# Optimization experiments

Measured on AMD Instinct MI355X. Metric: run time of the kernel, lower is better.

## Reference

```python
import jax, jax.numpy as jnp
import numpy as np

B, S, E, A = 4, 4096, 512, 64

def setup_inputs() -> dict:
    key = jax.random.key(0)
    ks = jax.random.split(key, 9)
    return {
        "query": jax.random.normal(ks[0], (B, S, E), dtype=jnp.float32),
        "key":   jax.random.normal(ks[1], (B, S, E), dtype=jnp.float32),
        "value": jax.random.normal(ks[2], (B, S, E), dtype=jnp.float32),
        "Wq": jax.random.normal(ks[3], (E, A), dtype=jnp.float32) / np.sqrt(E),
        "bq": jax.random.normal(ks[4], (A,), dtype=jnp.float32) * 0.01,
        "Wk": jax.random.normal(ks[5], (E, A), dtype=jnp.float32) / np.sqrt(E),
        "bk": jax.random.normal(ks[6], (A,), dtype=jnp.float32) * 0.01,
        "Wv": jax.random.normal(ks[7], (E, A), dtype=jnp.float32) / np.sqrt(E),
        "bv": jax.random.normal(ks[8], (A,), dtype=jnp.float32) * 0.01,
        "look_ahead_mask": 1,
    }

def reference(query, key, value, Wq, bq, Wk, bk, Wv, bv, look_ahead_mask):
    # Linear projections (torch Linear: x @ W^T + b; here W stored as [in,out])
    q = query @ Wq + bq            # [B,S,A]
    k = key   @ Wk + bk            # [B,S,A]
    v = value @ Wv + bv            # [B,S,A]
    scale = jnp.sqrt(jnp.asarray(A, dtype=q.dtype))
    qk = jnp.einsum('bsa,bta->bst', q, k) / scale   # [B,S,S]
    if look_ahead_mask:
        # faithful to source: MULTIPLICATIVE tril mask (not additive -inf)
        tril = jnp.tril(jnp.ones((qk.shape[-1], qk.shape[-1]), dtype=qk.dtype))
        qk = qk * tril
    attn = jax.nn.softmax(qk, axis=-1)              # [B,S,S]
    return jnp.einsum('bst,bta->bsa', attn, v)       # [B,S,A]
```

## Files before the change

### kernel.cpp

```cpp
#include <hip/hip_runtime.h>
#include <cstdint>

constexpr int BB = 4, SS = 4096, EE = 512, AA = 64;
constexpr int NT = 64;
constexpr int NSLOT = 272;

typedef __bf16 bf16x8 __attribute__((ext_vector_type(8)));
typedef float  f32x4  __attribute__((ext_vector_type(4)));
typedef float  f4     __attribute__((ext_vector_type(4)));
typedef unsigned short u16x4 __attribute__((ext_vector_type(4)));
typedef unsigned short u16x8 __attribute__((ext_vector_type(8)));

#define MFMA16(a, b, c) __builtin_amdgcn_mfma_f32_16x16x32_bf16((a), (b), (c), 0, 0, 0)

typedef const void __attribute__((address_space(1))) gvoid_t;
typedef void __attribute__((address_space(3))) lvoid_t;
__device__ __forceinline__ void gload16(const void* g, void* l) {
    __builtin_amdgcn_global_load_lds((gvoid_t*)g, (lvoid_t*)l, 16, 0, 0);
}

__device__ __forceinline__ unsigned short f2bf(float x) {
    union { float f; unsigned u; } v; v.f = x;
    unsigned r = v.u + 0x7fffu + ((v.u >> 16) & 1u);
    return (unsigned short)(r >> 16);
}
__device__ __forceinline__ float bf2f(unsigned short h) {
    union { unsigned u; float f; } v; v.u = ((unsigned)h) << 16;
    return v.f;
}
__device__ __forceinline__ unsigned short f2bfc(float x) {
    __bf16 h = (__bf16)x;
    return __builtin_bit_cast(unsigned short, h);
}
__device__ __forceinline__ bf16x8 as_bf16x8(u16x8 u) {
    union { u16x8 u; bf16x8 b; } v; v.u = u; return v.b;
}

__global__ void split_w_kernel(const float* __restrict__ Wq,
                               const float* __restrict__ Wk,
                               const float* __restrict__ Wv,
                               unsigned short* __restrict__ wt_h,
                               unsigned short* __restrict__ wt_l) {
    int idx = blockIdx.x * blockDim.x + threadIdx.x;
    if (idx >= 3 * EE * AA) return;
    int t = idx / (EE * AA);
    int rem = idx - t * (EE * AA);
    int k = rem >> 6;
    int n = rem & 63;
    const float* W = (t == 0) ? Wq : (t == 1) ? Wk : Wv;
    float x = W[k * AA + n];
    unsigned short h = f2bf(x);
    unsigned short l = f2bf(x - bf2f(h));
    int o = (t * AA + n) * EE + k;
    wt_h[o] = h;
    wt_l[o] = l;
}

__launch_bounds__(128)
__global__ void proj_kernel(const float* __restrict__ Xq,
                            const float* __restrict__ Xk,
                            const float* __restrict__ Xv,
                            const float* __restrict__ bq,
                            const float* __restrict__ bk,
                            const float* __restrict__ bv,
                            const unsigned short* __restrict__ wt_h,
                            const unsigned short* __restrict__ wt_l,
                            unsigned short* __restrict__ q_hi,
                            unsigned short* __restrict__ q_lo,
                            unsigned short* __restrict__ kv) {
    const int t = blockIdx.y;
    const float* X    = (t == 0) ? Xq : (t == 1) ? Xk : Xv;
    const float* bias = (t == 0) ? bq : (t == 1) ? bk : bv;
    const int row0 = blockIdx.x * 32;
    const int tid = threadIdx.x;
    const int lane = tid & 63, w = tid >> 6;
    const int l15 = lane & 15, l4 = lane >> 4;

    __shared__ __align__(16) char smem[24576];

    f32x4 acc[4];
#pragma unroll
    for (int j = 0; j < 4; ++j) acc[j] = (f32x4){0.f, 0.f, 0.f, 0.f};

    const unsigned short* wtH = wt_h + t * AA * EE;
    const unsigned short* wtL = wt_l + t * AA * EE;

    for (int kc0 = 0; kc0 < EE; kc0 += 64) {
#pragma unroll
        for (int s = 0; s < 4; ++s) {
            int r = s * 8 + (tid >> 4);
            int c4 = (tid & 15) ^ (r & 7);
            gload16(X + (size_t)(row0 + r) * EE + kc0 + c4 * 4,
                    smem + s * 2048 + tid * 16);
        }
#pragma unroll
        for (int s = 0; s < 4; ++s) {
            int n = s * 16 + (tid >> 3);
            int cg = (tid & 7) ^ (n & 7);
            gload16(wtH + n * EE + kc0 + cg * 8,
                    smem + 8192 + s * 2048 + tid * 16);
            gload16(wtL + n * EE + kc0 + cg * 8,
                    smem + 16384 + s * 2048 + tid * 16);
        }
        asm volatile("s_waitcnt vmcnt(0)" ::: "memory");
        __syncthreads();

#pragma unroll
        for (int kc = 0; kc < 2; ++kc) {
            int r = w * 16 + l15;
            int c4a = (kc * 8 + l4 * 2) ^ (r & 7);
            int c4b = (kc * 8 + l4 * 2 + 1) ^ (r & 7);
            f4 va = *(const f4*)(smem + r * 256 + c4a * 16);
            f4 vb = *(const f4*)(smem + r * 256 + c4b * 16);
            u16x8 ahu, alu;
#pragma unroll
            for (int jj = 0; jj < 4; ++jj) {
                __bf16 h0 = (__bf16)va[jj];
                ahu[jj] = __builtin_bit_cast(unsigned short, h0);
                alu[jj] = f2bfc(va[jj] - (float)h0);
                __bf16 h1 = (__bf16)vb[jj];
                ahu[jj + 4] = __builtin_bit_cast(unsigned short, h1);
                alu[jj + 4] = f2bfc(vb[jj] - (float)h1);
            }
            bf16x8 a_h = as_bf16x8(ahu), a_l = as_bf16x8(alu);
#pragma unroll
            for (int j = 0; j < 4; ++j) {
                int n = j * 16 + l15;
                int byteB = n * 128 + (((kc * 4 + l4) ^ (n & 7)) << 4);
                bf16x8 b_h = as_bf16x8(*(const u16x8*)(smem + 8192 + byteB));
                bf16x8 b_l = as_bf16x8(*(const u16x8*)(smem + 16384 + byteB));
                acc[j] = MFMA16(a_h, b_h, acc[j]);
                acc[j] = MFMA16(a_h, b_l, acc[j]);
                acc[j] = MFMA16(a_l, b_h, acc[j]);
            }
        }
        __syncthreads();
    }

    float* stage = (float*)smem;
#pragma unroll
    for (int j = 0; j < 4; ++j) {
        int n = j * 16 + l15;
        float bv_ = bias[n];
#pragma unroll
        for (int reg = 0; reg < 4; ++reg) {
            int r = w * 16 + l4 * 4 + reg;
            stage[r * 65 + n] = acc[j][reg] + bv_;
        }
    }
    __syncthreads();

    if (t == 0) {
        int row = tid >> 2, n0 = (tid & 3) * 16;
        u16x8 h0, l0, h1, l1;
#pragma unroll
        for (int k = 0; k < 8; ++k) {
            float v = stage[row * 65 + n0 + k] * 0.125f;
            __bf16 hh = (__bf16)v;
            h0[k] = __builtin_bit_cast(unsigned short, hh);
            l0[k] = f2bfc(v - (float)hh);
        }
#pragma unroll
        for (int k = 0; k < 8; ++k) {
            float v = stage[row * 65 + n0 + 8 + k] * 0.125f;
            __bf16 hh = (__bf16)v;
            h1[k] = __builtin_bit_cast(unsigned short, hh);
            l1[k] = f2bfc(v - (float)hh);
        }
        size_t o = (size_t)(row0 + row) * AA + n0;
        *(u16x8*)(q_hi + o) = h0; *(u16x8*)(q_hi + o + 8) = h1;
        *(u16x8*)(q_lo + o) = l0; *(u16x8*)(q_lo + o + 8) = l1;
    } else {
        const int bb = row0 >> 12, kt = (row0 & 4095) >> 6;
        const int hb = (row0 >> 5) & 1;
        const size_t base = ((size_t)(bb * NT + kt) << 14) + (t == 2 ? 8192 : 0);
        const int ff = tid >> 5;
#pragma unroll
        for (int p = 0; p < 2; ++p) {
            int lane2 = (tid & 31) * 2 + p;
            u16x8 h, l;
            int f;
            if (t == 1) {
                f = (ff >> 1) * 4 + 2 * hb + (ff & 1);
                int n0 = (f >> 2) * 32 + (lane2 >> 4) * 8;
                int tt = (f & 3) * 16 + (lane2 & 15);
                int sr = tt & 31;
#pragma unroll
                for (int jj = 0; jj < 8; ++jj) {
                    float v = stage[sr * 65 + n0 + jj];
                    __bf16 hh = (__bf16)v;
                    h[jj] = __builtin_bit_cast(unsigned short, hh);
                    l[jj] = f2bfc(v - (float)hh);
                }
            } else {
                f = 4 * hb + ff;
                int n = (f & 3) * 16 + (lane2 & 15);
                int tt0 = (lane2 >> 4) * 8;
#pragma unroll
                for (int jj = 0; jj < 8; ++jj) {
                    float v = stage[(tt0 + jj) * 65 + n];
                    __bf16 hh = (__bf16)v;
                    h[jj] = __builtin_bit_cast(unsigned short, hh);
                    l[jj] = f2bfc(v - (float)hh);
                }
            }
            size_t o = base + (size_t)f * 512 + lane2 * 8;
            *(u16x8*)(kv + o) = h;
            *(u16x8*)(kv + o + 4096) = l;
        }
    }
}

__launch_bounds__(64)
__global__ void sufv_kernel(const unsigned short* __restrict__ kv,
                            float* __restrict__ sufv) {
    const int b = blockIdx.x >> 6;
    const int a = blockIdx.x & 63;
    const int t = threadIdx.x;
    __shared__ float sums[64];
    const size_t tb = ((size_t)(b * NT + t) << 14) + 8192;
    const int j = a >> 4, l15i = a & 15;
    float s = 0.f;
#pragma unroll
    for (int c2 = 0; c2 < 2; ++c2) {
#pragma unroll
        for (int l4i = 0; l4i < 4; ++l4i) {
            size_t off = tb + (((c2 * 4 + j) * 64 + l4i * 16 + l15i) << 3);
            u16x8 h = *(const u16x8*)(kv + off);
            u16x8 l = *(const u16x8*)(kv + off + 4096);
#pragma unroll
            for (int q = 0; q < 8; ++q) s += bf2f(h[q]) + bf2f(l[q]);
        }
    }
    sums[t] = s;
    __syncthreads();
    float suf = 0.f;
    for (int jj = t + 1; jj < 64; ++jj) suf += sums[jj];
    sufv[((size_t)(b * 64 + a)) * 64 + t] = suf;
}

__launch_bounds__(512)
__global__ void attn_chunk_kernel(const unsigned short* __restrict__ q_hi,
                                  const unsigned short* __restrict__ q_lo,
                                  const unsigned short* __restrict__ kv,
                                  float* __restrict__ facc_part,
                                  float* __restrict__ l_part) {
    const int idx = (int)blockIdx.x;
    const int b = idx & 3;
    const int s = (NSLOT - 1) - (idx >> 2);
    int k = (int)sqrtf((float)s + 0.5f);
    while (k * k > s) --k;
    while ((k + 1) * (k + 1) <= s) ++k;
    int i, c;
    if (s < k * (k + 1)) { i = 2 * k - 1; c = s - k * k; }
    else                 { i = 2 * k;     c = s - k * (k + 1); }
    const int t_begin = c * 4;
    const int tmax = 2 * i + 2;
    const int t_end = (t_begin + 4 < tmax) ? t_begin + 4 : tmax;

    const int tid = threadIdx.x;
    const int lane = tid & 63, w = tid >> 6;
    const int l15 = lane & 15, l4 = lane >> 4;

    __shared__ __align__(16) unsigned short kvbuf[16384];
    __shared__ __align__(16) unsigned short plds[8][1024];

    bf16x8 qh[2], ql[2];
    {
        size_t qrow = (size_t)(b * SS + i * 128 + w * 16 + l15) * AA;
#pragma unroll
        for (int kc = 0; kc < 2; ++kc) {
            qh[kc] = as_bf16x8(*(const u16x8*)(q_hi + qrow + kc * 32 + l4 * 8));
            ql[kc] = as_bf16x8(*(const u16x8*)(q_lo + qrow + kc * 32 + l4 * 8));
        }
    }

    f32x4 facc[4];
#pragma unroll
    for (int j = 0; j < 4; ++j) facc[j] = (f32x4){0.f, 0.f, 0.f, 0.f};
    float lsum = 0.f;

    const char* lb = (const char*)kvbuf;
    const int qbase = i * 128 + w * 16;

    for (int kt = t_begin; kt < t_end; ++kt) {
        {
            const char* gt = (const char*)kv + (((size_t)(b * NT + kt)) << 15) + tid * 16;
            char* lw = (char*)kvbuf + tid * 16;
#pragma unroll
            for (int p = 0; p < 4; ++p) gload16(gt + p * 8192, lw + p * 8192);
        }
        asm volatile("s_waitcnt vmcnt(0)" ::: "memory");
        __syncthreads();

        f32x4 sc[4];
#pragma unroll
        for (int j = 0; j < 4; ++j) sc[j] = (f32x4){0.f, 0.f, 0.f, 0.f};
        __builtin_amdgcn_s_setprio(1);
#pragma unroll
        for (int kc = 0; kc < 2; ++kc) {
#pragma unroll
            for (int j2 = 0; j2 < 4; ++j2) {
                int f = kc * 4 + j2;
                bf16x8 h = as_bf16x8(*(const u16x8*)(lb + f * 1024 + lane * 16));
                bf16x8 l = as_bf16x8(*(const u16x8*)(lb + 8192 + f * 1024 + lane * 16));
                sc[j2] = MFMA16(h, qh[kc], sc[j2]);
                sc[j2] = MFMA16(l, qh[kc], sc[j2]);
                sc[j2] = MFMA16(h, ql[kc], sc[j2]);
            }
        }
        __builtin_amdgcn_s_setprio(0);

        const int dq = qbase - 64 * kt;
        const bool anyMask = (dq < 63);
#pragma unroll
        for (int j2 = 0; j2 < 4; ++j2) {
            u16x4 p4;
#pragma unroll
            for (int reg = 0; reg < 4; ++reg) {
                float sv_ = sc[j2][reg];
                if (anyMask) {
                    int tl = j2 * 16 + l4 * 4 + reg;
                    if (tl > dq + l15) sv_ = 0.f;
                }
                float p = __expf(sv_);
                lsum += p;
                p4[reg] = f2bf(p);
            }
            int byte = (l15 * 128 + j2 * 32 + l4 * 8) ^ ((l15 & 7) << 4);
            *(u16x4*)((char*)plds[w] + byte) = p4;
        }

        __builtin_amdgcn_s_setprio(1);
#pragma unroll
        for (int c2 = 0; c2 < 2; ++c2) {
            int byteA = (l15 * 128 + c2 * 64 + l4 * 16) ^ ((l15 & 7) << 4);
            bf16x8 pf = as_bf16x8(*(const u16x8*)((const char*)plds[w] + byteA));
#pragma unroll
            for (int j = 0; j < 4; ++j) {
                int f = c2 * 4 + j;
                bf16x8 vh = as_bf16x8(*(const u16x8*)(lb + 16384 + f * 1024 + lane * 16));
                bf16x8 vl = as_bf16x8(*(const u16x8*)(lb + 24576 + f * 1024 + lane * 16));
                facc[j] = MFMA16(pf, vh, facc[j]);
                facc[j] = MFMA16(pf, vl, facc[j]);
            }
        }
        __builtin_amdgcn_s_setprio(0);

        if (kt + 1 < t_end) __syncthreads();
    }

    {
        float rs = lsum;
        rs += __shfl_xor(rs, 16);
        rs += __shfl_xor(rs, 32);
        const size_t slot = (size_t)b * NSLOT + s;
        if (l4 == 0)
            l_part[slot * 128 + w * 16 + l15] = rs;

        float* fp = facc_part + slot * 8192;
#pragma unroll
        for (int j = 0; j < 4; ++j) {
#pragma unroll
            for (int reg = 0; reg < 4; ++reg) {
                int row = w * 16 + l4 * 4 + reg, a = j * 16 + l15;
                fp[row * 64 + a] = facc[j][reg];
            }
        }
    }
}

__launch_bounds__(256)
__global__ void combine_kernel(const float* __restrict__ facc_part,
                               const float* __restrict__ l_part,
                               const float* __restrict__ sufv,
                               float* __restrict__ out) {
    const int i64 = blockIdx.x;
    const int b = blockIdx.y;
    const int tid = threadIdx.x;
    const int i128 = i64 >> 1;
    const int nch = (i128 >> 1) + 1;
    const int k2 = i128 >> 1;
    const int C = (i128 & 1) ? (k2 + 1) * (k2 + 1) : k2 * (k2 + 1);
    const size_t slot0 = (size_t)b * NSLOT + C;
    const int rbase = (i64 & 1) * 64;
    __shared__ float linv[64];
    __shared__ float sv[64];
    if (tid < 64) {
        float l = 64.0f * (float)(NT - 2 * i128 - 2);
        for (int cc = 0; cc < nch; ++cc)
            l += l_part[(slot0 + cc) * 128 + rbase + tid];
        linv[tid] = 1.f / l;
        sv[tid] = sufv[((size_t)(b * 64 + tid)) * 64 + (2 * i128 + 1)];
    }
    __syncthreads();
    float* ob = out + ((size_t)(b * SS + i64 * 64)) * AA;
#pragma unroll
    for (int k = 0; k < 4; ++k) {
        int e = (tid + k * 256) * 4;
        int row = e >> 6, a = e & 63;
        f4 acc = {sv[a], sv[a + 1], sv[a + 2], sv[a + 3]};
        for (int cc = 0; cc < nch; ++cc) {
            f4 v = *(const f4*)(facc_part + (slot0 + cc) * 8192 + (rbase + row) * 64 + a);
            acc += v;
        }
        acc *= linv[row];
        *(f4*)(ob + e) = acc;
    }
}

extern "C" void kernel_launch(void* const* d_in, const int* in_sizes, int n_in,
                              void* d_out, int out_size, void* d_ws, size_t ws_size,
                              hipStream_t stream) {
    const float* query = (const float*)d_in[0];
    const float* key   = (const float*)d_in[1];
    const float* value = (const float*)d_in[2];
    const float* Wq    = (const float*)d_in[3];
    const float* bq    = (const float*)d_in[4];
    const float* Wk    = (const float*)d_in[5];
    const float* bk    = (const float*)d_in[6];
    const float* Wv    = (const float*)d_in[7];
    const float* bv    = (const float*)d_in[8];

    char* ws = (char*)d_ws;
    const size_t MB = 1u << 20;
    unsigned short* q_hi = (unsigned short*)(ws + 0 * MB);
    unsigned short* q_lo = (unsigned short*)(ws + 2 * MB);
    unsigned short* kv   = (unsigned short*)(ws + 4 * MB);
    float* sufv      = (float*)(ws + 12 * MB);
    float* l_part    = (float*)(ws + 13 * MB);
    float* facc_part = (float*)(ws + 14 * MB);
    unsigned short* wt_h = (unsigned short*)(ws + 52 * MB);
    unsigned short* wt_l = wt_h + 3 * AA * EE;

    split_w_kernel<<<(3 * EE * AA + 255) / 256, 256, 0, stream>>>(Wq, Wk, Wv, wt_h, wt_l);
    proj_kernel<<<dim3(BB * SS / 32, 3), 128, 0, stream>>>(
        query, key, value, bq, bk, bv, wt_h, wt_l, q_hi, q_lo, kv);
    sufv_kernel<<<BB * AA, 64, 0, stream>>>(kv, sufv);
    attn_chunk_kernel<<<dim3(4 * NSLOT, 1), 512, 0, stream>>>(
        q_hi, q_lo, kv, facc_part, l_part);
    combine_kernel<<<dim3(NT, BB), 256, 0, stream>>>(facc_part, l_part, sufv, (float*)d_out);
}
```

Before: 94.75 us.

## Double K-chunk in projection and batch two KV tiles per sync in attention

The projection kernel now stages 128-wide K chunks per iteration, doubling its shared memory to halve the number of load/sync rounds. The attention kernel loads two consecutive KV tiles into a doubled LDS buffer with one wait and barrier, then processes both through a macro-expanded tile body. The aim is fewer global-load round trips and barriers. In exchange LDS use per block grows, which may reduce occupancy.

Measured after the change: 95.34 us. About the same (+0.6%).

```diff
diff --git a/kernel.cpp b/kernel.cpp
--- a/kernel.cpp
+++ b/kernel.cpp
@@ -76,7 +76,7 @@
     const int lane = tid & 63, w = tid >> 6;
     const int l15 = lane & 15, l4 = lane >> 4;
 
-    __shared__ __align__(16) char smem[24576];
+    __shared__ __align__(16) char smem[49152];
 
     f32x4 acc[4];
 #pragma unroll
@@ -85,33 +85,33 @@
     const unsigned short* wtH = wt_h + t * AA * EE;
     const unsigned short* wtL = wt_l + t * AA * EE;
 
-    for (int kc0 = 0; kc0 < EE; kc0 += 64) {
-#pragma unroll
-        for (int s = 0; s < 4; ++s) {
-            int r = s * 8 + (tid >> 4);
-            int c4 = (tid & 15) ^ (r & 7);
-            gload16(X + (size_t)(row0 + r) * EE + kc0 + c4 * 4,
-                    smem + s * 2048 + tid * 16);
-        }
-#pragma unroll
-        for (int s = 0; s < 4; ++s) {
-            int n = s * 16 + (tid >> 3);
-            int cg = (tid & 7) ^ (n & 7);
-            gload16(wtH + n * EE + kc0 + cg * 8,
-                    smem + 8192 + s * 2048 + tid * 16);
-            gload16(wtL + n * EE + kc0 + cg * 8,
-                    smem + 16384 + s * 2048 + tid * 16);
+    for (int kc0 = 0; kc0 < EE; kc0 += 128) {
+#pragma unroll
+        for (int s = 0; s < 8; ++s) {
+            int e = s * 128 + tid;
+            int r = e >> 5, g = e & 31;
+            int cg = g ^ (r & 7);
+            gload16(X + (size_t)(row0 + r) * EE + kc0 + cg * 4,
+                    smem + e * 16);
+        }
+#pragma unroll
+        for (int s = 0; s < 8; ++s) {
+            int e = s * 128 + tid;
+            int n = e >> 4, g = e & 15;
+            int cg = g ^ (n & 7);
+            gload16(wtH + n * EE + kc0 + cg * 8, smem + 16384 + e * 16);
+            gload16(wtL + n * EE + kc0 + cg * 8, smem + 32768 + e * 16);
         }
         asm volatile("s_waitcnt vmcnt(0)" ::: "memory");
         __syncthreads();
 
 #pragma unroll
-        for (int kc = 0; kc < 2; ++kc) {
+        for (int kc = 0; kc < 4; ++kc) {
             int r = w * 16 + l15;
-            int c4a = (kc * 8 + l4 * 2) ^ (r & 7);
-            int c4b = (kc * 8 + l4 * 2 + 1) ^ (r & 7);
-            f4 va = *(const f4*)(smem + r * 256 + c4a * 16);
-            f4 vb = *(const f4*)(smem + r * 256 + c4b * 16);
+            int g0 = (kc * 8 + l4 * 2) ^ (r & 7);
+            int g1 = (kc * 8 + l4 * 2 + 1) ^ (r & 7);
+            f4 va = *(const f4*)(smem + r * 512 + g0 * 16);
+            f4 vb = *(const f4*)(smem + r * 512 + g1 * 16);
             u16x8 ahu, alu;
 #pragma unroll
             for (int jj = 0; jj < 4; ++jj) {
@@ -126,9 +126,9 @@
 #pragma unroll
             for (int j = 0; j < 4; ++j) {
                 int n = j * 16 + l15;
-                int byteB = n * 128 + (((kc * 4 + l4) ^ (n & 7)) << 4);
-                bf16x8 b_h = as_bf16x8(*(const u16x8*)(smem + 8192 + byteB));
-                bf16x8 b_l = as_bf16x8(*(const u16x8*)(smem + 16384 + byteB));
+                int byteB = n * 256 + (((kc * 4 + l4) ^ (n & 7)) << 4);
+                bf16x8 b_h = as_bf16x8(*(const u16x8*)(smem + 16384 + byteB));
+                bf16x8 b_l = as_bf16x8(*(const u16x8*)(smem + 32768 + byteB));
                 acc[j] = MFMA16(a_h, b_h, acc[j]);
                 acc[j] = MFMA16(a_h, b_l, acc[j]);
                 acc[j] = MFMA16(a_l, b_h, acc[j]);
@@ -238,6 +238,56 @@
     for (int jj = t + 1; jj < 64; ++jj) suf += sums[jj];
     sufv[((size_t)(b * 64 + a)) * 64 + t] = suf;
 }
+
+#define ATTN_TILE(LB, KT)                                                      \
+  do {                                                                         \
+    const char* lb = (LB);                                                     \
+    f32x4 sc[4];                                                               \
+    _Pragma("unroll") for (int j = 0; j < 4; ++j)                              \
+        sc[j] = (f32x4){0.f, 0.f, 0.f, 0.f};                                   \
+    __builtin_amdgcn_s_setprio(1);                                             \
+    _Pragma("unroll") for (int kc = 0; kc < 2; ++kc) {                         \
+      _Pragma("unroll") for (int j2 = 0; j2 < 4; ++j2) {                       \
+        int f = kc * 4 + j2;                                                   \
+        bf16x8 h = as_bf16x8(*(const u16x8*)(lb + f * 1024 + lane * 16));      \
+        bf16x8 l = as_bf16x8(*(const u16x8*)(lb + 8192 + f * 1024 + lane * 16));\
+        sc[j2] = MFMA16(h, qh[kc], sc[j2]);                                    \
+        sc[j2] = MFMA16(l, qh[kc], sc[j2]);                                    \
+        sc[j2] = MFMA16(h, ql[kc], sc[j2]);                                    \
+      }                                                                        \
+    }                                                                          \
+    __builtin_amdgcn_s_setprio(0);                                             \
+    const int dq = qbase - 64 * (KT);                                          \
+    const bool anyMask = (dq < 63);                                            \
+    _Pragma("unroll") for (int j2 = 0; j2 < 4; ++j2) {                         \
+      u16x4 p4;                                                                \
+      _Pragma("unroll") for (int reg = 0; reg < 4; ++reg) {                    \
+        float sv_ = sc[j2][reg];                                               \
+        if (anyMask) {                                                         \
+          int tl = j2 * 16 + l4 * 4 + reg;                                     \
+          if (tl > dq + l15) sv_ = 0.f;                                        \
+        }                                                                      \
+        float p = __expf(sv_);                                                 \
+        lsum += p;                                                             \
+        p4[reg] = f2bf(p);                                                     \
+      }                                                                        \
+      int byte = (l15 * 128 + j2 * 32 + l4 * 8) ^ ((l15 & 7) << 4);            \
+      *(u16x4*)((char*)plds[w] + byte) = p4;                                   \
+    }                                                                          \
+    __builtin_amdgcn_s_setprio(1);                                             \
+    _Pragma("unroll") for (int c2 = 0; c2 < 2; ++c2) {                         \
+      int byteA = (l15 * 128 + c2 * 64 + l4 * 16) ^ ((l15 & 7) << 4);          \
+      bf16x8 pf = as_bf16x8(*(const u16x8*)((const char*)plds[w] + byteA));    \
+      _Pragma("unroll") for (int j = 0; j < 4; ++j) {                          \
+        int f = c2 * 4 + j;                                                    \
+        bf16x8 vh = as_bf16x8(*(const u16x8*)(lb + 16384 + f * 1024 + lane * 16));\
+        bf16x8 vl = as_bf16x8(*(const u16x8*)(lb + 24576 + f * 1024 + lane * 16));\
+        facc[j] = MFMA16(pf, vh, facc[j]);                                     \
+        facc[j] = MFMA16(pf, vl, facc[j]);                                     \
+      }                                                                        \
+    }                                                                          \
+    __builtin_amdgcn_s_setprio(0);                                             \
+  } while (0)
 
 __launch_bounds__(512)
 __global__ void attn_chunk_kernel(const unsigned short* __restrict__ q_hi,
@@ -262,7 +312,7 @@
     const int lane = tid & 63, w = tid >> 6;
     const int l15 = lane & 15, l4 = lane >> 4;
 
-    __shared__ __align__(16) unsigned short kvbuf[16384];
+    __shared__ __align__(16) unsigned short kvbuf[2][16384];
     __shared__ __align__(16) unsigned short plds[8][1024];
 
     bf16x8 qh[2], ql[2];
@@ -280,74 +330,28 @@
     for (int j = 0; j < 4; ++j) facc[j] = (f32x4){0.f, 0.f, 0.f, 0.f};
     float lsum = 0.f;
 
-    const char* lb = (const char*)kvbuf;
     const int qbase = i * 128 + w * 16;
-
-    for (int kt = t_begin; kt < t_end; ++kt) {
+    const char* gbase = (const char*)kv + (((size_t)(b * NT)) << 15) + tid * 16;
+
+    for (int kt = t_begin; kt < t_end; kt += 2) {
+        const int np = (kt + 1 < t_end) ? 2 : 1;
         {
-            const char* gt = (const char*)kv + (((size_t)(b * NT + kt)) << 15) + tid * 16;
-            char* lw = (char*)kvbuf + tid * 16;
+            const char* gt = gbase + (((size_t)kt) << 15);
+            char* lw = (char*)kvbuf[0] + tid * 16;
 #pragma unroll
             for (int p = 0; p < 4; ++p) gload16(gt + p * 8192, lw + p * 8192);
+            if (np == 2) {
+#pragma unroll
+                for (int p = 4; p < 8; ++p) gload16(gt + p * 8192, lw + p * 8192);
+            }
         }
         asm volatile("s_waitcnt vmcnt(0)" ::: "memory");
         __syncthreads();
 
-        f32x4 sc[4];
-#pragma unroll
-        for (int j = 0; j < 4; ++j) sc[j] = (f32x4){0.f, 0.f, 0.f, 0.f};
-        __builtin_amdgcn_s_setprio(1);
-#pragma unroll
-        for (int kc = 0; kc < 2; ++kc) {
-#pragma unroll
-            for (int j2 = 0; j2 < 4; ++j2) {
-                int f = kc * 4 + j2;
-                bf16x8 h = as_bf16x8(*(const u16x8*)(lb + f * 1024 + lane * 16));
-                bf16x8 l = as_bf16x8(*(const u16x8*)(lb + 8192 + f * 1024 + lane * 16));
-                sc[j2] = MFMA16(h, qh[kc], sc[j2]);
-                sc[j2] = MFMA16(l, qh[kc], sc[j2]);
-                sc[j2] = MFMA16(h, ql[kc], sc[j2]);
-            }
-        }
-        __builtin_amdgcn_s_setprio(0);
-
-        const int dq = qbase - 64 * kt;
-        const bool anyMask = (dq < 63);
-#pragma unroll
-        for (int j2 = 0; j2 < 4; ++j2) {
-            u16x4 p4;
-#pragma unroll
-            for (int reg = 0; reg < 4; ++reg) {
-                float sv_ = sc[j2][reg];
-                if (anyMask) {
-                    int tl = j2 * 16 + l4 * 4 + reg;
-                    if (tl > dq + l15) sv_ = 0.f;
-                }
-                float p = __expf(sv_);
-                lsum += p;
-                p4[reg] = f2bf(p);
-            }
-            int byte = (l15 * 128 + j2 * 32 + l4 * 8) ^ ((l15 & 7) << 4);
-            *(u16x4*)((char*)plds[w] + byte) = p4;
-        }
-
-        __builtin_amdgcn_s_setprio(1);
-#pragma unroll
-        for (int c2 = 0; c2 < 2; ++c2) {
-            int byteA = (l15 * 128 + c2 * 64 + l4 * 16) ^ ((l15 & 7) << 4);
-            bf16x8 pf = as_bf16x8(*(const u16x8*)((const char*)plds[w] + byteA));
-#pragma unroll
-            for (int j = 0; j < 4; ++j) {
-                int f = c2 * 4 + j;
-                bf16x8 vh = as_bf16x8(*(const u16x8*)(lb + 16384 + f * 1024 + lane * 16));
-                bf16x8 vl = as_bf16x8(*(const u16x8*)(lb + 24576 + f * 1024 + lane * 16));
-                facc[j] = MFMA16(pf, vh, facc[j]);
-                facc[j] = MFMA16(pf, vl, facc[j]);
-            }
-        }
-        __builtin_amdgcn_s_setprio(0);
-
-        if (kt + 1 < t_end) __syncthreads();
+        ATTN_TILE((const char*)kvbuf[0], kt);
+        if (np == 2) ATTN_TILE((const char*)kvbuf[1], kt + 1);
+
+        if (kt + 2 < t_end) __syncthreads();
     }
 
     {
```
